# Performance work log

Hardware: AMD Instinct MI355X
Metric: run time of the kernel (lower is better)

The kernel has to match this reference:

```python
import jax, jax.numpy as jnp
import numpy as np

B, N, D, K = 8, 8192, 256, 3


def setup_inputs() -> dict:
    key = jax.random.key(0)
    k0, k1, k2, k3 = jax.random.split(key, 4)
    basic_units = jax.random.normal(k0, (B, N, D), dtype=jnp.float32)
    # learned params: offset/modulation linear weights (K, D) and conv weight (D, D, K)
    offset_w = jax.random.normal(k1, (K, D), dtype=jnp.float32) * 0.02
    mod_w = jax.random.normal(k2, (K, D), dtype=jnp.float32) * 0.1
    fan_in = D * K
    weight = jax.random.normal(k3, (D, D, K), dtype=jnp.float32) * np.sqrt(2.0 / fan_in)
    return {"basic_units": basic_units, "offset_w": offset_w, "mod_w": mod_w, "weight": weight}


def reference(basic_units, offset_w, mod_w, weight):
    b, n, d = basic_units.shape
    k = weight.shape[2]
    # offsets and modulation per token per kernel tap: (B, N, K)
    offset = jnp.einsum('bnd,kd->bnk', basic_units, offset_w)
    modulation = jax.nn.sigmoid(jnp.einsum('bnd,kd->bnk', basic_units, mod_w))
    # base sampling position i + k - K//2, perturbed by data-dependent offset
    base = (jnp.arange(n)[:, None] + jnp.arange(k)[None, :] - k // 2).astype(basic_units.dtype)  # (N, K)
    pos = base[None, :, :] + offset  # (B, N, K)
    valid = (pos >= 0) & (pos < n)
    floor_f = jnp.clip(jnp.floor(pos), 0, n - 1)
    fi = floor_f.astype(jnp.int32)               # (B, N, K)
    ci = jnp.minimum(fi + 1, n - 1)
    w_ceil = pos - floor_f
    w_floor = 1.0 - w_ceil

    def gather(idx):
        # x[b, idx[b, i, k], :] -> (B, N, K, D)
        return jnp.take_along_axis(basic_units, idx.reshape(b, n * k, 1), axis=1).reshape(b, n, k, d)

    interp = w_floor[..., None] * gather(fi) + w_ceil[..., None] * gather(ci)  # (B, N, K, D)
    # modulate, zero out-of-range taps, then per-tap matmul summed over taps
    modulated = interp * (modulation * valid.astype(interp.dtype))[..., None]
    out = jnp.einsum('dek,bike->bid', weight, modulated)
    return out
```

## Files before the change

kernel.cpp:

```cpp
#include <hip/hip_runtime.h>
#include <hip/hip_bf16.h>
#include <cstdint>


#define N_TOK 8192
#define DIM   256
#define KW    768
#define BM    128
#define BN    128
#define BK    32

typedef unsigned short u16;
typedef __attribute__((ext_vector_type(4))) float    floatx4;
typedef __attribute__((ext_vector_type(8))) __bf16   bf16x8;
typedef __attribute__((ext_vector_type(8))) u16      ushortx8;

__device__ __forceinline__ u16 f32_to_bf16_rne(float f) {
    uint32_t u = __float_as_uint(f);
    u += 0x7fffu + ((u >> 16) & 1u);
    return (u16)(u >> 16);
}

__global__ __launch_bounds__(256) void coef_kernel(
    const float* __restrict__ x, const float* __restrict__ offw,
    const float* __restrict__ modw, int4* __restrict__ coef)
{
    const int wave = threadIdx.x >> 6;
    const int lane = threadIdx.x & 63;
    const int t = blockIdx.x * 4 + wave;

    const float4 xv = ((const float4*)(x + (size_t)t * DIM))[lane];
    float s[6];
#pragma unroll
    for (int k = 0; k < 3; ++k) {
        float4 wv = ((const float4*)(offw + k * DIM))[lane];
        s[k]     = xv.x * wv.x + xv.y * wv.y + xv.z * wv.z + xv.w * wv.w;
        float4 mv = ((const float4*)(modw + k * DIM))[lane];
        s[3 + k] = xv.x * mv.x + xv.y * mv.y + xv.z * mv.z + xv.w * mv.w;
    }
#pragma unroll
    for (int d = 1; d < 64; d <<= 1) {
#pragma unroll
        for (int i = 0; i < 6; ++i) s[i] += __shfl_xor(s[i], d, 64);
    }
    if (lane < 3) {
        const int k = lane;
        const int n = t & (N_TOK - 1);
        float pos   = (float)(n + k - 1) + s[k];
        bool  valid = (pos >= 0.0f) && (pos < (float)N_TOK);
        float ff = floorf(pos);
        ff = fminf(fmaxf(ff, 0.0f), (float)(N_TOK - 1));
        int   fi = (int)ff;
        int   ci = min(fi + 1, N_TOK - 1);
        float wc = pos - ff;
        float m  = valid ? (1.0f / (1.0f + expf(-s[3 + k]))) : 0.0f;
        coef[t * 3 + k] = make_int4(fi, ci,
                                    __float_as_int((1.0f - wc) * m),
                                    __float_as_int(wc * m));
    }
}

__global__ __launch_bounds__(256) void packw_kernel(
    const float* __restrict__ W, u16* __restrict__ WB)
{
    const int d = blockIdx.x;
    const int e = threadIdx.x;
#pragma unroll
    for (int k = 0; k < 3; ++k)
        WB[d * KW + k * DIM + e] = f32_to_bf16_rne(W[d * KW + e * 3 + k]);
}

__global__ __launch_bounds__(256) void deform_gemm_kernel(
    const float* __restrict__ x, const u16* __restrict__ WB,
    const int4* __restrict__ coef, float* __restrict__ out)
{
    __shared__ __align__(16) u16 As[2][BM * 40];
    __shared__ __align__(16) u16 Bs[2][BN * 40];

    const int tid  = threadIdx.x;
    const int wave = tid >> 6;
    const int lane = tid & 63;

    const int raw   = blockIdx.x;
    const int xcd   = raw & 7;
    const int lidx  = raw >> 3;
    const int mtile = xcd * ((65536 / BM) / 8) + (lidx >> 1);
    const int ntile = lidx & 1;

    const int t0 = mtile * BM;
    const int n0 = ntile * BN;
    const float* xb = x + (size_t)(t0 / N_TOK) * N_TOK * DIM;

    const int tl = tid >> 1;
    const int eh = tid & 1;
    const int wm = (wave & 1) * 64;
    const int wn = (wave >> 1) * 64;
    const int lrow = lane & 15;
    const int lq   = lane >> 4;

    const int4 cc0 = coef[(size_t)(t0 + tl) * 3 + 0];
    const int4 cc1 = coef[(size_t)(t0 + tl) * 3 + 1];
    const int4 cc2 = coef[(size_t)(t0 + tl) * 3 + 2];

    float4 pf[4], pc[4];
    uint4  pb0, pb1;
    float  wA, wC;

    auto loadg = [&](int kk) {
        const int tap = kk >> 3;
        const int4 c = (tap == 0) ? cc0 : (tap == 1 ? cc1 : cc2);
        const int e0 = (kk & 7) * 32 + eh * 16;
        wA = __int_as_float(c.z);
        wC = __int_as_float(c.w);
        const float4* rowf = (const float4*)(xb + (size_t)c.x * DIM + e0);
        const float4* rowc = (const float4*)(xb + (size_t)c.y * DIM + e0);
#pragma unroll
        for (int j = 0; j < 4; ++j) { pf[j] = rowf[j]; pc[j] = rowc[j]; }
        const uint4* g = (const uint4*)(WB + (size_t)(n0 + tl) * KW + kk * BK + eh * 16);
        pb0 = g[0];
        pb1 = g[1];
    };

    auto packstore = [&](int buf) {
        uint32_t p[8];
#pragma unroll
        for (int j = 0; j < 4; ++j) {
            float r0 = wA * pf[j].x + wC * pc[j].x;
            float r1 = wA * pf[j].y + wC * pc[j].y;
            float r2 = wA * pf[j].z + wC * pc[j].z;
            float r3 = wA * pf[j].w + wC * pc[j].w;
            p[j * 2 + 0] = __builtin_amdgcn_perm(__float_as_uint(r1), __float_as_uint(r0), 0x07060302u);
            p[j * 2 + 1] = __builtin_amdgcn_perm(__float_as_uint(r3), __float_as_uint(r2), 0x07060302u);
        }
        uint4* adst = (uint4*)&As[buf][tl * 40 + eh * 16];
        adst[0] = make_uint4(p[0], p[1], p[2], p[3]);
        adst[1] = make_uint4(p[4], p[5], p[6], p[7]);
        uint4* bdst = (uint4*)&Bs[buf][tl * 40 + eh * 16];
        bdst[0] = pb0;
        bdst[1] = pb1;
    };

    loadg(0);
    packstore(0);
    loadg(1);

    floatx4 acc[4][4];
#pragma unroll
    for (int i = 0; i < 4; ++i)
#pragma unroll
        for (int j = 0; j < 4; ++j) acc[i][j] = (floatx4){0.f, 0.f, 0.f, 0.f};

    __syncthreads();

    for (int kk = 0; kk < 24; ++kk) {
        const int cur = kk & 1;
        bf16x8 af[4], bfv[4];
#pragma unroll
        for (int i = 0; i < 4; ++i)
            af[i] = __builtin_bit_cast(bf16x8, *(const ushortx8*)&As[cur][(wm + i * 16 + lrow) * 40 + lq * 8]);
#pragma unroll
        for (int j = 0; j < 4; ++j)
            bfv[j] = __builtin_bit_cast(bf16x8, *(const ushortx8*)&Bs[cur][(wn + j * 16 + lrow) * 40 + lq * 8]);
        if (kk < 23) packstore(cur ^ 1);
        if (kk < 22) loadg(kk + 2);
#pragma unroll
        for (int i = 0; i < 4; ++i)
#pragma unroll
            for (int j = 0; j < 4; ++j)
                acc[i][j] = __builtin_amdgcn_mfma_f32_16x16x32_bf16(af[i], bfv[j], acc[i][j], 0, 0, 0);
        __syncthreads();
    }

#pragma unroll
    for (int i = 0; i < 4; ++i) {
#pragma unroll
        for (int r = 0; r < 4; ++r) {
            const int token = t0 + wm + i * 16 + lq * 4 + r;
            float* op = out + (size_t)token * DIM + n0 + wn + lrow;
#pragma unroll
            for (int j = 0; j < 4; ++j) op[j * 16] = acc[i][j][r];
        }
    }
}

extern "C" void kernel_launch(void* const* d_in, const int* in_sizes, int n_in,
                              void* d_out, int out_size, void* d_ws, size_t ws_size,
                              hipStream_t stream)
{
    const float* x    = (const float*)d_in[0];
    const float* offw = (const float*)d_in[1];
    const float* modw = (const float*)d_in[2];
    const float* W    = (const float*)d_in[3];
    float* out = (float*)d_out;

    const int tot_tok = 8 * N_TOK;
    int4* coef = (int4*)d_ws;
    u16*  WB   = (u16*)((char*)d_ws + (size_t)tot_tok * 3 * 16);

    coef_kernel<<<tot_tok / 4, 256, 0, stream>>>(x, offw, modw, coef);
    packw_kernel<<<DIM, 256, 0, stream>>>(W, WB);
    deform_gemm_kernel<<<(tot_tok / BM) * (DIM / BN), 256, 0, stream>>>(x, WB, coef, out);
}
```

Before: 184.1 us.

## Cover all output columns per block so each gathered row is interpolated once

Reshapes the GEMM tile from 128x128 to 64x256 and moves to 512-thread blocks, so every block computes the full output width. Each token's deformable interpolation (two gathered rows blended by coefficients) is now loaded and computed once instead of once per column tile. Load and interpolation work is spread across 8 lanes per row, and each wave computes a 32x64 sub-tile. The cost is a smaller M tile per block, and the 512-thread launch bound with a minimum of 4 blocks per CU may limit registers.

```diff
diff --git a/kernel.cpp b/kernel.cpp
--- a/kernel.cpp
+++ b/kernel.cpp
@@ -6,8 +6,8 @@
 #define N_TOK 8192
 #define DIM   256
 #define KW    768
-#define BM    128
-#define BN    128
+#define BM    64
+#define BN    256
 #define BK    32
 
 typedef unsigned short u16;
@@ -70,7 +70,7 @@
         WB[d * KW + k * DIM + e] = f32_to_bf16_rne(W[d * KW + e * 3 + k]);
 }
 
-__global__ __launch_bounds__(256) void deform_gemm_kernel(
+__global__ __launch_bounds__(512, 4) void deform_gemm_kernel(
     const float* __restrict__ x, const u16* __restrict__ WB,
     const int4* __restrict__ coef, float* __restrict__ out)
 {
@@ -84,16 +84,16 @@
     const int raw   = blockIdx.x;
     const int xcd   = raw & 7;
     const int lidx  = raw >> 3;
-    const int mtile = xcd * ((65536 / BM) / 8) + (lidx >> 1);
-    const int ntile = lidx & 1;
-
+    const int mtile = xcd * 128 + lidx;
     const int t0 = mtile * BM;
-    const int n0 = ntile * BN;
     const float* xb = x + (size_t)(t0 / N_TOK) * N_TOK * DIM;
 
-    const int tl = tid >> 1;
-    const int eh = tid & 1;
-    const int wm = (wave & 1) * 64;
+    const int tl  = tid >> 3;
+    const int sub = tid & 7;
+    const int br = tid >> 1;
+    const int bh = tid & 1;
+
+    const int wm = (wave & 1) * 32;
     const int wn = (wave >> 1) * 64;
     const int lrow = lane & 15;
     const int lq   = lane >> 4;
@@ -102,40 +102,32 @@
     const int4 cc1 = coef[(size_t)(t0 + tl) * 3 + 1];
     const int4 cc2 = coef[(size_t)(t0 + tl) * 3 + 2];
 
-    float4 pf[4], pc[4];
+    float4 pf, pc;
     uint4  pb0, pb1;
     float  wA, wC;
 
     auto loadg = [&](int kk) {
         const int tap = kk >> 3;
         const int4 c = (tap == 0) ? cc0 : (tap == 1 ? cc1 : cc2);
-        const int e0 = (kk & 7) * 32 + eh * 16;
+        const int e0 = (kk & 7) * 32 + sub * 4;
         wA = __int_as_float(c.z);
         wC = __int_as_float(c.w);
-        const float4* rowf = (const float4*)(xb + (size_t)c.x * DIM + e0);
-        const float4* rowc = (const float4*)(xb + (size_t)c.y * DIM + e0);
-#pragma unroll
-        for (int j = 0; j < 4; ++j) { pf[j] = rowf[j]; pc[j] = rowc[j]; }
-        const uint4* g = (const uint4*)(WB + (size_t)(n0 + tl) * KW + kk * BK + eh * 16);
+        pf = *(const float4*)(xb + (size_t)c.x * DIM + e0);
+        pc = *(const float4*)(xb + (size_t)c.y * DIM + e0);
+        const uint4* g = (const uint4*)(WB + (size_t)br * KW + kk * BK + bh * 16);
         pb0 = g[0];
         pb1 = g[1];
     };
 
     auto packstore = [&](int buf) {
-        uint32_t p[8];
-#pragma unroll
-        for (int j = 0; j < 4; ++j) {
-            float r0 = wA * pf[j].x + wC * pc[j].x;
-            float r1 = wA * pf[j].y + wC * pc[j].y;
-            float r2 = wA * pf[j].z + wC * pc[j].z;
-            float r3 = wA * pf[j].w + wC * pc[j].w;
-            p[j * 2 + 0] = __builtin_amdgcn_perm(__float_as_uint(r1), __float_as_uint(r0), 0x07060302u);
-            p[j * 2 + 1] = __builtin_amdgcn_perm(__float_as_uint(r3), __float_as_uint(r2), 0x07060302u);
-        }
-        uint4* adst = (uint4*)&As[buf][tl * 40 + eh * 16];
-        adst[0] = make_uint4(p[0], p[1], p[2], p[3]);
-        adst[1] = make_uint4(p[4], p[5], p[6], p[7]);
-        uint4* bdst = (uint4*)&Bs[buf][tl * 40 + eh * 16];
+        float r0 = wA * pf.x + wC * pc.x;
+        float r1 = wA * pf.y + wC * pc.y;
+        float r2 = wA * pf.z + wC * pc.z;
+        float r3 = wA * pf.w + wC * pc.w;
+        uint32_t p0 = __builtin_amdgcn_perm(__float_as_uint(r1), __float_as_uint(r0), 0x07060302u);
+        uint32_t p1 = __builtin_amdgcn_perm(__float_as_uint(r3), __float_as_uint(r2), 0x07060302u);
+        *(uint2*)&As[buf][tl * 40 + sub * 4] = make_uint2(p0, p1);
+        uint4* bdst = (uint4*)&Bs[buf][br * 40 + bh * 16];
         bdst[0] = pb0;
         bdst[1] = pb1;
     };
@@ -144,9 +136,9 @@
     packstore(0);
     loadg(1);
 
-    floatx4 acc[4][4];
+    floatx4 acc[2][4];
 #pragma unroll
-    for (int i = 0; i < 4; ++i)
+    for (int i = 0; i < 2; ++i)
 #pragma unroll
         for (int j = 0; j < 4; ++j) acc[i][j] = (floatx4){0.f, 0.f, 0.f, 0.f};
 
@@ -154,9 +146,9 @@
 
     for (int kk = 0; kk < 24; ++kk) {
         const int cur = kk & 1;
-        bf16x8 af[4], bfv[4];
+        bf16x8 af[2], bfv[4];
 #pragma unroll
-        for (int i = 0; i < 4; ++i)
+        for (int i = 0; i < 2; ++i)
             af[i] = __builtin_bit_cast(bf16x8, *(const ushortx8*)&As[cur][(wm + i * 16 + lrow) * 40 + lq * 8]);
 #pragma unroll
         for (int j = 0; j < 4; ++j)
@@ -164,7 +156,7 @@
         if (kk < 23) packstore(cur ^ 1);
         if (kk < 22) loadg(kk + 2);
 #pragma unroll
-        for (int i = 0; i < 4; ++i)
+        for (int i = 0; i < 2; ++i)
 #pragma unroll
             for (int j = 0; j < 4; ++j)
                 acc[i][j] = __builtin_amdgcn_mfma_f32_16x16x32_bf16(af[i], bfv[j], acc[i][j], 0, 0, 0);
@@ -172,11 +164,11 @@
     }
 
 #pragma unroll
-    for (int i = 0; i < 4; ++i) {
+    for (int i = 0; i < 2; ++i) {
 #pragma unroll
         for (int r = 0; r < 4; ++r) {
             const int token = t0 + wm + i * 16 + lq * 4 + r;
-            float* op = out + (size_t)token * DIM + n0 + wn + lrow;
+            float* op = out + (size_t)token * DIM + wn + lrow;
 #pragma unroll
             for (int j = 0; j < 4; ++j) op[j * 16] = acc[i][j][r];
         }
@@ -199,5 +191,5 @@
 
     coef_kernel<<<tot_tok / 4, 256, 0, stream>>>(x, offw, modw, coef);
     packw_kernel<<<DIM, 256, 0, stream>>>(W, WB);
-    deform_gemm_kernel<<<(tot_tok / BM) * (DIM / BN), 256, 0, stream>>>(x, WB, coef, out);
+    deform_gemm_kernel<<<tot_tok / BM, 512, 0, stream>>>(x, WB, coef, out);
 }
```

After: 176.8 us. 1.04x faster.
